# Performance work log

Hardware: AMD Instinct MI355X
Metric: run time of the kernel (lower is better)

Reference implementation:

```python
import jax, jax.numpy as jnp
import numpy as np

V, H, O = 50257, 1024, 1024
B, T = 64, 256

def setup_inputs() -> dict:
    key = jax.random.key(0)
    ks = jax.random.split(key, 8)
    s = 1.0 / np.sqrt(H)
    return {
        "input": jax.random.randint(ks[0], (B, T), 0, V),
        "hidden": jnp.zeros((B, H), jnp.float32),
        "emb": jax.random.normal(ks[1], (V, H), jnp.float32),
        "Wi": jax.random.uniform(ks[2], (H, H), jnp.float32, -s, s),
        "bi": jax.random.uniform(ks[3], (H,), jnp.float32, -s, s),
        "Wh": jax.random.uniform(ks[4], (H, H), jnp.float32, -s, s),
        "bh": jax.random.uniform(ks[5], (H,), jnp.float32, -s, s),
        "Wo": jax.random.uniform(ks[6], (H, O), jnp.float32, -s, s),
        "bo": jax.random.uniform(ks[7], (O,), jnp.float32, -s, s),
    }

def reference(input, hidden, emb, Wi, bi, Wh, bh, Wo, bo):
    # embedded: [B, T, H]; precompute the input-to-hidden projection for all steps
    embedded = emb[input]
    ix = jnp.einsum('bth,hk->tbk', embedded, Wi) + bi  # [T, B, H]

    def step(h, ix_t):
        h = jnp.tanh(ix_t + h @ Wh + bh)
        out = h @ Wo + bo
        return h, out

    hidden, outs = jax.lax.scan(step, hidden, ix)  # outs: [T, B, O]
    output_seq = jnp.transpose(outs, (1, 0, 2))    # [B, T, O]
    return output_seq, hidden
```

## Files before the change

### kernel.cpp

```cpp
#include <hip/hip_runtime.h>

typedef unsigned short u16;
typedef unsigned long long u64;
typedef short v8s __attribute__((ext_vector_type(8)));
typedef float v4f __attribute__((ext_vector_type(4)));

__device__ __forceinline__ u16 f2bf(float x) {
    union { float f; unsigned u; } v; v.f = x;
    unsigned r = v.u + 0x7fffu + ((v.u >> 16) & 1u);
    return (u16)(r >> 16);
}

__global__ __launch_bounds__(256) void convert_w(
    const float* __restrict__ Wi, const float* __restrict__ Wh,
    const float* __restrict__ Wo, u16* __restrict__ wi_t,
    u16* __restrict__ wh_t, u16* __restrict__ wo_t) {
    const float* src; u16* dst;
    if (blockIdx.y == 0)      { src = Wi; dst = wi_t; }
    else if (blockIdx.y == 1) { src = Wh; dst = wh_t; }
    else                      { src = Wo; dst = wo_t; }
    int k0 = (blockIdx.x & 31) * 32;
    int n0 = (blockIdx.x >> 5) * 32;
    __shared__ float tile[32][33];
    int t = threadIdx.x;
    {
        int kl = t >> 3, nl4 = (t & 7) * 4;
        float4 v = *(const float4*)(src + (size_t)(k0 + kl) * 1024 + n0 + nl4);
        tile[kl][nl4 + 0] = v.x; tile[kl][nl4 + 1] = v.y;
        tile[kl][nl4 + 2] = v.z; tile[kl][nl4 + 3] = v.w;
    }
    __syncthreads();
    {
        int nl = t >> 3, kl4 = (t & 7) * 4;
        ushort4 o;
        o.x = f2bf(tile[kl4 + 0][nl]); o.y = f2bf(tile[kl4 + 1][nl]);
        o.z = f2bf(tile[kl4 + 2][nl]); o.w = f2bf(tile[kl4 + 3][nl]);
        *(ushort4*)(dst + (size_t)(n0 + nl) * 1024 + k0 + kl4) = o;
    }
}

__global__ __launch_bounds__(256) void gather_emb(
    const int* __restrict__ input, const float* __restrict__ emb,
    u16* __restrict__ Aemb) {
    int r = blockIdx.x * 4 + (threadIdx.x >> 6);
    int lane = threadIdx.x & 63;
    int b = r & 63, t = r >> 6;
    int idx = input[b * 256 + t];
    const float* s = emb + (size_t)idx * 1024;
    u16* d = Aemb + (size_t)r * 1024;
#pragma unroll
    for (int i = 0; i < 4; i++) {
        float4 v = *(const float4*)(s + i * 256 + lane * 4);
        ushort4 o;
        o.x = f2bf(v.x); o.y = f2bf(v.y); o.z = f2bf(v.z); o.w = f2bf(v.w);
        *(ushort4*)(d + i * 256 + lane * 4) = o;
    }
}

__global__ __launch_bounds__(256) void gemm_bias(
    const u16* __restrict__ A, const u16* __restrict__ Bt,
    const float* __restrict__ bias, float* __restrict__ out, int mode) {
    __shared__ u16 lA[128 * 40];
    __shared__ u16 lB[128 * 40];
    const int tid = threadIdx.x;
    const int w = tid >> 6, lane = tid & 63;
    const int l15 = lane & 15, quad = lane >> 4;
    const int m0 = blockIdx.x * 128, n0 = blockIdx.y * 128;
    const int wm = (w & 1) * 64, wn = (w >> 1) * 64;
    const int srow = tid >> 1, shalf = tid & 1;
    const u16* gA = A + (size_t)(m0 + srow) * 1024 + shalf * 16;
    const u16* gB = Bt + (size_t)(n0 + srow) * 1024 + shalf * 16;
    v4f zero = {0.f, 0.f, 0.f, 0.f};
    v4f acc[4][4];
#pragma unroll
    for (int i = 0; i < 4; i++)
#pragma unroll
        for (int j = 0; j < 4; j++) acc[i][j] = zero;

    uint4 ra0 = *(const uint4*)gA;
    uint4 ra1 = *(const uint4*)(gA + 8);
    uint4 rb0 = *(const uint4*)gB;
    uint4 rb1 = *(const uint4*)(gB + 8);

    for (int kt = 0; kt < 32; ++kt) {
        __syncthreads();
        *(uint4*)(lA + srow * 40 + shalf * 16) = ra0;
        *(uint4*)(lA + srow * 40 + shalf * 16 + 8) = ra1;
        *(uint4*)(lB + srow * 40 + shalf * 16) = rb0;
        *(uint4*)(lB + srow * 40 + shalf * 16 + 8) = rb1;
        __syncthreads();
        if (kt < 31) {
            const u16* pA = gA + (kt + 1) * 32;
            const u16* pB = gB + (kt + 1) * 32;
            ra0 = *(const uint4*)pA; ra1 = *(const uint4*)(pA + 8);
            rb0 = *(const uint4*)pB; rb1 = *(const uint4*)(pB + 8);
        }
        v8s af[4], bfv[4];
#pragma unroll
        for (int mt = 0; mt < 4; mt++)
            af[mt] = *(const v8s*)(lA + (wm + mt * 16 + l15) * 40 + quad * 8);
#pragma unroll
        for (int nt = 0; nt < 4; nt++)
            bfv[nt] = *(const v8s*)(lB + (wn + nt * 16 + l15) * 40 + quad * 8);
#pragma unroll
        for (int mt = 0; mt < 4; mt++)
#pragma unroll
            for (int nt = 0; nt < 4; nt++)
                acc[mt][nt] = __builtin_amdgcn_mfma_f32_16x16x32_bf16(
                    af[mt], bfv[nt], acc[mt][nt], 0, 0, 0);
    }
#pragma unroll
    for (int nt = 0; nt < 4; nt++) {
        int coln = n0 + wn + nt * 16 + l15;
        float bv = bias[coln];
#pragma unroll
        for (int mt = 0; mt < 4; mt++) {
            int rbase = m0 + wm + mt * 16 + quad * 4;
#pragma unroll
            for (int r = 0; r < 4; r++) {
                int row = rbase + r;
                int orow = mode ? ((row & 63) * 256 + (row >> 6)) : row;
                out[(size_t)orow * 1024 + coln] = acc[mt][nt][r] + bv;
            }
        }
    }
}

__global__ __launch_bounds__(256, 1) void rnn_step_all(
    const u16* __restrict__ wh_t, const float* __restrict__ bh,
    const float* __restrict__ ix, u64* __restrict__ h_buf64,
    u16* __restrict__ h_all, float* __restrict__ out_tail,
    unsigned* __restrict__ flags) {
    const int tid = threadIdx.x, w = tid >> 6, lane = tid & 63;
    const int g = blockIdx.x, gb = g & 3, gc = g >> 2;
    const int quad = lane >> 4, l15 = lane & 15;
    const int col = gc * 64 + w * 16 + l15;
    __shared__ u16 hts[16 * 1032];

    v8s bfr[32];
#pragma unroll
    for (int kc = 0; kc < 32; kc++)
        bfr[kc] = *(const v8s*)(wh_t + (size_t)col * 1024 + kc * 32 + quad * 8);
    const float bhv = bh[col];
    const int mrow0 = gb * 16 + quad * 4;
    const int srow = tid >> 4, sseg = tid & 15;

    for (int t = 0; t < 256; t++) {
        float ixv[4];
        {
            const float* ixp = ix + ((size_t)t * 64 + mrow0) * 1024 + col;
#pragma unroll
            for (int r = 0; r < 4; r++) ixv[r] = ixp[(size_t)r * 1024];
        }
        v4f acc = {0.f, 0.f, 0.f, 0.f};
        if (t > 0) {
            if (tid == 0) {
                const unsigned* fp = flags + t * 4 + gb;
                int cnt = 0;
                while (__hip_atomic_load(fp, __ATOMIC_RELAXED,
                                         __HIP_MEMORY_SCOPE_AGENT) < 16u) {
                    if (++cnt > (1 << 20)) break;
                }
            }
            __syncthreads();
            const u64* hsrc =
                h_buf64 + (size_t)(t & 1) * 16384 + (gb * 16 + srow) * 256;
            u64 tmp[16];
#pragma unroll
            for (int i = 0; i < 16; i++)
                tmp[i] = __hip_atomic_load(hsrc + sseg + i * 16,
                                           __ATOMIC_RELAXED,
                                           __HIP_MEMORY_SCOPE_AGENT);
#pragma unroll
            for (int i = 0; i < 16; i++)
                *(u64*)(hts + srow * 1032 + (sseg + i * 16) * 4) = tmp[i];
            __syncthreads();
#pragma unroll
            for (int kc = 0; kc < 32; kc++) {
                v8s a = *(const v8s*)(hts + l15 * 1032 + kc * 32 + quad * 8);
                acc = __builtin_amdgcn_mfma_f32_16x16x32_bf16(a, bfr[kc], acc,
                                                              0, 0, 0);
            }
        }
        float hv[4]; u16 hb[4];
#pragma unroll
        for (int r = 0; r < 4; r++) {
            float pre = acc[r] + ixv[r] + bhv;
            hv[r] = tanhf(pre);
            hb[r] = f2bf(hv[r]);
        }
        u64* hdst = h_buf64 + (size_t)((t + 1) & 1) * 16384;
#pragma unroll
        for (int r = 0; r < 4; r++) {
            unsigned own = hb[r];
            unsigned other = __shfl_xor(own, 1);
            unsigned p = own | (other << 16);
            unsigned p2 = __shfl_xor(p, 2);
            if ((lane & 3) == 0) {
                u64 q = (u64)p | ((u64)p2 << 32);
                __hip_atomic_store(hdst + (mrow0 + r) * 256 + (col >> 2), q,
                                   __ATOMIC_RELAXED, __HIP_MEMORY_SCOPE_AGENT);
            }
        }
        __syncthreads();
        if (tid == 0)
            __hip_atomic_fetch_add(flags + (t + 1) * 4 + gb, 1u,
                                   __ATOMIC_RELAXED, __HIP_MEMORY_SCOPE_AGENT);
        u16* hall = h_all + (size_t)t * 65536;
#pragma unroll
        for (int r = 0; r < 4; r++) {
            hall[(size_t)(mrow0 + r) * 1024 + col] = hb[r];
            if (t == 255) out_tail[(mrow0 + r) * 1024 + col] = hv[r];
        }
    }
}

extern "C" void kernel_launch(void* const* d_in, const int* in_sizes, int n_in,
                              void* d_out, int out_size, void* d_ws,
                              size_t ws_size, hipStream_t stream) {
    const int*   input = (const int*)d_in[0];
    const float* emb = (const float*)d_in[2];
    const float* Wi  = (const float*)d_in[3];
    const float* bi  = (const float*)d_in[4];
    const float* Wh  = (const float*)d_in[5];
    const float* bh  = (const float*)d_in[6];
    const float* Wo  = (const float*)d_in[7];
    const float* bo  = (const float*)d_in[8];
    float* out = (float*)d_out;
    char* ws = (char*)d_ws;

    u16* wi_t  = (u16*)(ws);
    u16* wh_t  = (u16*)(ws + (2ull << 20));
    u16* wo_t  = (u16*)(ws + (4ull << 20));
    u16* Aemb  = (u16*)(ws + (6ull << 20));
    u64* h_buf = (u64*)(ws + (38ull << 20));
    unsigned* flags = (unsigned*)(ws + (38ull << 20) + (512ull << 10));

    float* ix = out;
    float* out_tail = out + 16777216ull;

    hipMemsetAsync(flags, 0, 8192, stream);
    convert_w<<<dim3(1024, 3), 256, 0, stream>>>(Wi, Wh, Wo, wi_t, wh_t, wo_t);
    gather_emb<<<4096, 256, 0, stream>>>(input, emb, Aemb);
    gemm_bias<<<dim3(128, 8), 256, 0, stream>>>(Aemb, wi_t, bi, ix, 0);
    rnn_step_all<<<64, 256, 0, stream>>>(wh_t, bh, ix, h_buf, Aemb, out_tail,
                                         flags);
    gemm_bias<<<dim3(128, 8), 256, 0, stream>>>(Aemb, wo_t, bo, out, 1);
}
```

Before: 1.055 ms.

## Replace flag-counter barrier with sentinel-polled per-step hidden buffers

Drops the per-step atomic flag counter and single-thread spin-plus-barrier. Each step's hidden state now goes to its own slot in a full-history buffer, memset beforehand to a sentinel pattern. Values are stored bitwise-inverted so a real value never matches the sentinel, and consumers poll their own words until none match. The next step's loads are issued early, the separate h_all write is gone because the output GEMM reads the inverted history directly, and tanhf becomes a fast exp-based tanh. The cost is an extra 32MB memset and a small risk that a genuine inverted value collides with the sentinel.

```diff
diff --git a/kernel.cpp b/kernel.cpp
--- a/kernel.cpp
+++ b/kernel.cpp
@@ -1,14 +1,28 @@
 #include <hip/hip_runtime.h>
 
 typedef unsigned short u16;
+typedef unsigned int u32;
 typedef unsigned long long u64;
 typedef short v8s __attribute__((ext_vector_type(8)));
 typedef float v4f __attribute__((ext_vector_type(4)));
+
+#define SENT 0xAAAAAAAAu
 
 __device__ __forceinline__ u16 f2bf(float x) {
     union { float f; unsigned u; } v; v.f = x;
     unsigned r = v.u + 0x7fffu + ((v.u >> 16) & 1u);
     return (u16)(r >> 16);
+}
+
+__device__ __forceinline__ float fast_tanh(float x) {
+    float ax = fabsf(x);
+    float z = __expf(-2.0f * ax);
+    float r = __fdividef(1.0f - z, 1.0f + z);
+    return copysignf(r, x);
+}
+
+__device__ __forceinline__ uint4 xor4(uint4 v, unsigned m) {
+    v.x ^= m; v.y ^= m; v.z ^= m; v.w ^= m; return v;
 }
 
 __global__ __launch_bounds__(256) void convert_w(
@@ -59,7 +73,8 @@
 
 __global__ __launch_bounds__(256) void gemm_bias(
     const u16* __restrict__ A, const u16* __restrict__ Bt,
-    const float* __restrict__ bias, float* __restrict__ out, int mode) {
+    const float* __restrict__ bias, float* __restrict__ out, int mode,
+    int inv) {
     __shared__ u16 lA[128 * 40];
     __shared__ u16 lB[128 * 40];
     const int tid = threadIdx.x;
@@ -68,6 +83,7 @@
     const int m0 = blockIdx.x * 128, n0 = blockIdx.y * 128;
     const int wm = (w & 1) * 64, wn = (w >> 1) * 64;
     const int srow = tid >> 1, shalf = tid & 1;
+    const unsigned xm = inv ? 0xFFFFFFFFu : 0u;
     const u16* gA = A + (size_t)(m0 + srow) * 1024 + shalf * 16;
     const u16* gB = Bt + (size_t)(n0 + srow) * 1024 + shalf * 16;
     v4f zero = {0.f, 0.f, 0.f, 0.f};
@@ -84,8 +100,8 @@
 
     for (int kt = 0; kt < 32; ++kt) {
         __syncthreads();
-        *(uint4*)(lA + srow * 40 + shalf * 16) = ra0;
-        *(uint4*)(lA + srow * 40 + shalf * 16 + 8) = ra1;
+        *(uint4*)(lA + srow * 40 + shalf * 16) = xor4(ra0, xm);
+        *(uint4*)(lA + srow * 40 + shalf * 16 + 8) = xor4(ra1, xm);
         *(uint4*)(lB + srow * 40 + shalf * 16) = rb0;
         *(uint4*)(lB + srow * 40 + shalf * 16 + 8) = rb1;
         __syncthreads();
@@ -128,9 +144,8 @@
 
 __global__ __launch_bounds__(256, 1) void rnn_step_all(
     const u16* __restrict__ wh_t, const float* __restrict__ bh,
-    const float* __restrict__ ix, u64* __restrict__ h_buf64,
-    u16* __restrict__ h_all, float* __restrict__ out_tail,
-    unsigned* __restrict__ flags) {
+    const float* __restrict__ ix, u64* __restrict__ hsteps,
+    float* __restrict__ out_tail) {
     const int tid = threadIdx.x, w = tid >> 6, lane = tid & 63;
     const int g = blockIdx.x, gb = g & 3, gc = g >> 2;
     const int quad = lane >> 4, l15 = lane & 15;
@@ -144,6 +159,9 @@
     const float bhv = bh[col];
     const int mrow0 = gb * 16 + quad * 4;
     const int srow = tid >> 4, sseg = tid & 15;
+    const int soff = (gb * 16 + srow) * 256 + sseg;
+
+    u64 tmp[16];
 
     for (int t = 0; t < 256; t++) {
         float ixv[4];
@@ -154,26 +172,26 @@
         }
         v4f acc = {0.f, 0.f, 0.f, 0.f};
         if (t > 0) {
-            if (tid == 0) {
-                const unsigned* fp = flags + t * 4 + gb;
-                int cnt = 0;
-                while (__hip_atomic_load(fp, __ATOMIC_RELAXED,
-                                         __HIP_MEMORY_SCOPE_AGENT) < 16u) {
-                    if (++cnt > (1 << 20)) break;
-                }
-            }
-            __syncthreads();
-            const u64* hsrc =
-                h_buf64 + (size_t)(t & 1) * 16384 + (gb * 16 + srow) * 256;
-            u64 tmp[16];
+            const u64* hsrc = hsteps + (size_t)(t - 1) * 16384 + soff;
+            int guard = 0;
+            while (true) {
+                u32 pend = 0;
+#pragma unroll
+                for (int i = 0; i < 16; i++)
+                    if ((u32)tmp[i] == SENT || (u32)(tmp[i] >> 32) == SENT)
+                        pend |= 1u << i;
+                if (!pend || guard > (1 << 16)) break;
+                ++guard;
+#pragma unroll
+                for (int i = 0; i < 16; i++)
+                    if (pend & (1u << i))
+                        tmp[i] = __hip_atomic_load(hsrc + i * 16,
+                                                   __ATOMIC_RELAXED,
+                                                   __HIP_MEMORY_SCOPE_AGENT);
+            }
 #pragma unroll
             for (int i = 0; i < 16; i++)
-                tmp[i] = __hip_atomic_load(hsrc + sseg + i * 16,
-                                           __ATOMIC_RELAXED,
-                                           __HIP_MEMORY_SCOPE_AGENT);
-#pragma unroll
-            for (int i = 0; i < 16; i++)
-                *(u64*)(hts + srow * 1032 + (sseg + i * 16) * 4) = tmp[i];
+                *(u64*)(hts + srow * 1032 + (sseg + i * 16) * 4) = ~tmp[i];
             __syncthreads();
 #pragma unroll
             for (int kc = 0; kc < 32; kc++) {
@@ -186,32 +204,34 @@
 #pragma unroll
         for (int r = 0; r < 4; r++) {
             float pre = acc[r] + ixv[r] + bhv;
-            hv[r] = tanhf(pre);
+            hv[r] = fast_tanh(pre);
             hb[r] = f2bf(hv[r]);
         }
-        u64* hdst = h_buf64 + (size_t)((t + 1) & 1) * 16384;
+        u64* hdst = hsteps + (size_t)t * 16384;
 #pragma unroll
         for (int r = 0; r < 4; r++) {
-            unsigned own = hb[r];
-            unsigned other = __shfl_xor(own, 1);
-            unsigned p = own | (other << 16);
-            unsigned p2 = __shfl_xor(p, 2);
+            u32 own = hb[r];
+            u32 other = __shfl_xor(own, 1);
+            u32 p = own | (other << 16);
+            u32 p2 = __shfl_xor(p, 2);
             if ((lane & 3) == 0) {
                 u64 q = (u64)p | ((u64)p2 << 32);
-                __hip_atomic_store(hdst + (mrow0 + r) * 256 + (col >> 2), q,
+                __hip_atomic_store(hdst + (mrow0 + r) * 256 + (col >> 2), ~q,
                                    __ATOMIC_RELAXED, __HIP_MEMORY_SCOPE_AGENT);
             }
         }
+        if (t == 255) {
+#pragma unroll
+            for (int r = 0; r < 4; r++)
+                out_tail[(mrow0 + r) * 1024 + col] = hv[r];
+        } else {
+            const u64* nsrc = hsteps + (size_t)t * 16384 + soff;
+#pragma unroll
+            for (int i = 0; i < 16; i++)
+                tmp[i] = __hip_atomic_load(nsrc + i * 16, __ATOMIC_RELAXED,
+                                           __HIP_MEMORY_SCOPE_AGENT);
+        }
         __syncthreads();
-        if (tid == 0)
-            __hip_atomic_fetch_add(flags + (t + 1) * 4 + gb, 1u,
-                                   __ATOMIC_RELAXED, __HIP_MEMORY_SCOPE_AGENT);
-        u16* hall = h_all + (size_t)t * 65536;
-#pragma unroll
-        for (int r = 0; r < 4; r++) {
-            hall[(size_t)(mrow0 + r) * 1024 + col] = hb[r];
-            if (t == 255) out_tail[(mrow0 + r) * 1024 + col] = hv[r];
-        }
     }
 }
 
@@ -233,17 +253,16 @@
     u16* wh_t  = (u16*)(ws + (2ull << 20));
     u16* wo_t  = (u16*)(ws + (4ull << 20));
     u16* Aemb  = (u16*)(ws + (6ull << 20));
-    u64* h_buf = (u64*)(ws + (38ull << 20));
-    unsigned* flags = (unsigned*)(ws + (38ull << 20) + (512ull << 10));
+    u64* hsteps = (u64*)Aemb;
 
     float* ix = out;
     float* out_tail = out + 16777216ull;
 
-    hipMemsetAsync(flags, 0, 8192, stream);
     convert_w<<<dim3(1024, 3), 256, 0, stream>>>(Wi, Wh, Wo, wi_t, wh_t, wo_t);
     gather_emb<<<4096, 256, 0, stream>>>(input, emb, Aemb);
-    gemm_bias<<<dim3(128, 8), 256, 0, stream>>>(Aemb, wi_t, bi, ix, 0);
-    rnn_step_all<<<64, 256, 0, stream>>>(wh_t, bh, ix, h_buf, Aemb, out_tail,
-                                         flags);
-    gemm_bias<<<dim3(128, 8), 256, 0, stream>>>(Aemb, wo_t, bo, out, 1);
-}
+    gemm_bias<<<dim3(128, 8), 256, 0, stream>>>(Aemb, wi_t, bi, ix, 0, 0);
+    hipMemsetAsync(hsteps, 0xAA, (32ull << 20), stream);
+    rnn_step_all<<<64, 256, 0, stream>>>(wh_t, bh, ix, hsteps, out_tail);
+    gemm_bias<<<dim3(128, 8), 256, 0, stream>>>((const u16*)hsteps, wo_t, bo,
+                                                out, 1, 1);
+}
```

New measurement: 1.635 ms. 1.55x slower.
